# Kernel tuning notes

Hardware: AMD Instinct MI355X
Metric: run time of the kernel (lower is better)

Reference implementation:

```python
import jax, jax.numpy as jnp
import numpy as np

NUM_HEADS = 16
FUTURE_FRAMES = 2
DIM = 1024


def setup_inputs() -> dict:
    key = jax.random.key(0)
    kx, kqkv, kp, kb = jax.random.split(key, 4)
    B, T = 2, 2048
    x = jax.random.normal(kx, (B, T, DIM), dtype=jnp.float32)
    # torch Linear weights stored transposed for direct x @ W use
    w_qkv = jax.random.normal(kqkv, (DIM, 3 * DIM), dtype=jnp.float32) * (DIM ** -0.5)
    w_proj = jax.random.normal(kp, (DIM, DIM), dtype=jnp.float32) * (DIM ** -0.5)
    b_proj = jax.random.normal(kb, (DIM,), dtype=jnp.float32) * 0.01
    return {"x": x, "w_qkv": w_qkv, "w_proj": w_proj, "b_proj": b_proj}


def reference(x, w_qkv, w_proj, b_proj):
    B, T, dim = x.shape
    H = NUM_HEADS
    hd = dim // H
    qkv = x @ w_qkv                                    # (B, T, 3*dim)
    q, k, v = jnp.split(qkv, 3, axis=-1)
    # (B, H, T, hd)
    q = q.reshape(B, T, H, hd).transpose(0, 2, 1, 3)
    k = k.reshape(B, T, H, hd).transpose(0, 2, 1, 3)
    v = v.reshape(B, T, H, hd).transpose(0, 2, 1, 3)
    scale = hd ** -0.5
    scores = jnp.einsum('bhqd,bhkd->bhqk', q, k) * scale
    # banded mask: query i may attend keys j with i <= j <= i + future_frames
    i = jnp.arange(T)[:, None]
    j = jnp.arange(T)[None, :]
    allowed = (j >= i) & (j <= i + FUTURE_FRAMES)       # (T, T)
    scores = jnp.where(allowed[None, None], scores, -jnp.inf)
    attn = jax.nn.softmax(scores, axis=-1)
    out = jnp.einsum('bhqk,bhkd->bhqd', attn, v)        # (B, H, T, hd)
    out = out.transpose(0, 2, 1, 3).reshape(B, T, dim)
    return out @ w_proj + b_proj
```

## Files before the change

kernel.cpp:

```cpp
#include <hip/hip_runtime.h>
#include <hip/hip_bf16.h>
#include <cstdint>
#include <cstddef>

#define T_SEQ 2048
#define NBATCH 2
#define DIMSZ 1024
#define NHEAD 16
#define HDIM 64

typedef float f32x4 __attribute__((ext_vector_type(4)));
typedef short bf16x8 __attribute__((ext_vector_type(8)));

__device__ __forceinline__ void gld_lds16(const __hip_bfloat16* g, __hip_bfloat16* l) {
    __builtin_amdgcn_global_load_lds(
        (const __attribute__((address_space(1))) unsigned int*)g,
        (__attribute__((address_space(3))) unsigned int*)l,
        16, 0, 0);
}

__device__ __forceinline__ float bf2f(unsigned short u) {
    union { unsigned int i; float f; } c; c.i = (unsigned int)u << 16; return c.f;
}

__global__ __launch_bounds__(256) void prep(
    const float* __restrict__ x,      __hip_bfloat16* __restrict__ xb,
    const float* __restrict__ wqkv,   __hip_bfloat16* __restrict__ wqkvT,
    const float* __restrict__ wproj,  __hip_bfloat16* __restrict__ wprojT)
{
    __shared__ float tile[32][33];
    const int b = blockIdx.x;
    if (b < 4096) {
        int i = (b * 256 + threadIdx.x) * 4;
        float4 v = *(const float4*)(x + i);
        union { __hip_bfloat16 h[4]; ushort4 u; } pk;
        pk.h[0] = __hip_bfloat16(v.x); pk.h[1] = __hip_bfloat16(v.y);
        pk.h[2] = __hip_bfloat16(v.z); pk.h[3] = __hip_bfloat16(v.w);
        *(ushort4*)(xb + i) = pk.u;
        return;
    }
    const float* in; __hip_bfloat16* out; int R, C, c0, r0;
    if (b < 7168) {
        int bb = b - 4096; in = wqkv; out = wqkvT; R = 1024; C = 3072;
        c0 = (bb % 96) * 32; r0 = (bb / 96) * 32;
    } else {
        int bb = b - 7168; in = wproj; out = wprojT; R = 1024; C = 1024;
        c0 = (bb & 31) * 32; r0 = (bb >> 5) * 32;
    }
    const int tx = threadIdx.x & 31, ty = threadIdx.x >> 5;
#pragma unroll
    for (int p = 0; p < 32; p += 8)
        tile[ty + p][tx] = in[(size_t)(r0 + ty + p) * C + c0 + tx];
    __syncthreads();
#pragma unroll
    for (int p = 0; p < 32; p += 8)
        out[(size_t)(c0 + ty + p) * R + r0 + tx] = __hip_bfloat16(tile[tx][ty + p]);
}

__global__ __launch_bounds__(256) void gemm_bt_128(
    const __hip_bfloat16* __restrict__ A,
    const __hip_bfloat16* __restrict__ Bt,
    __hip_bfloat16* __restrict__ C,
    int M, int N, int K)
{
    __shared__ __align__(16) __hip_bfloat16 As[2 * 128 * 32];
    __shared__ __align__(16) __hip_bfloat16 Bs[2 * 128 * 32];

    const int tid  = threadIdx.x;
    const int wv   = tid >> 6;
    const int lane = tid & 63;
    const int bn   = blockIdx.x, bm = blockIdx.y;
    const int wm   = wv >> 1, wn = wv & 1;

    f32x4 acc[4][4] = {};

    const int srow = lane >> 2;
    const int scol = (lane & 3) * 8;

    const __hip_bfloat16* Ag = A  + (size_t)(bm * 128) * K;
    const __hip_bfloat16* Bg = Bt + (size_t)(bn * 128) * K;

    const int fm = lane & 15;
    const int fq = (lane >> 4) * 8;

    for (int kk = 0; kk < K; kk += 64) {
#pragma unroll
        for (int kh = 0; kh < 2; ++kh)
#pragma unroll
            for (int it = 0; it < 2; ++it) {
                int row = (it * 4 + wv) * 16 + srow;
                gld_lds16(Ag + (size_t)row * K + kk + kh * 32 + scol,
                          As + kh * 4096 + row * 32 + scol);
                gld_lds16(Bg + (size_t)row * K + kk + kh * 32 + scol,
                          Bs + kh * 4096 + row * 32 + scol);
            }
        __syncthreads();

#pragma unroll
        for (int kh = 0; kh < 2; ++kh) {
            bf16x8 af[4], bfr[4];
#pragma unroll
            for (int i = 0; i < 4; ++i)
                af[i] = *(const bf16x8*)(As + kh * 4096 + (wm * 64 + i * 16 + fm) * 32 + fq);
#pragma unroll
            for (int j = 0; j < 4; ++j)
                bfr[j] = *(const bf16x8*)(Bs + kh * 4096 + (wn * 64 + j * 16 + fm) * 32 + fq);
#pragma unroll
            for (int i = 0; i < 4; ++i)
#pragma unroll
                for (int j = 0; j < 4; ++j)
                    acc[i][j] = __builtin_amdgcn_mfma_f32_16x16x32_bf16(af[i], bfr[j], acc[i][j], 0, 0, 0);
        }
        __syncthreads();
    }

    const int fcol  = lane & 15;
    const int frow4 = (lane >> 4) * 4;
    const int cm0 = bm * 128 + wm * 64;
    const int cn0 = bn * 128 + wn * 64;
#pragma unroll
    for (int j = 0; j < 4; ++j) {
        int col = cn0 + j * 16 + fcol;
#pragma unroll
        for (int i = 0; i < 4; ++i)
#pragma unroll
            for (int r = 0; r < 4; ++r) {
                int row = cm0 + i * 16 + frow4 + r;
                C[(size_t)row * N + col] = __hip_bfloat16(acc[i][j][r]);
            }
    }
}

__global__ __launch_bounds__(256) void gemm_bt_64(
    const __hip_bfloat16* __restrict__ A,
    const __hip_bfloat16* __restrict__ Bt,
    const float* __restrict__ bias,
    float* __restrict__ C,
    int M, int N, int K)
{
    __shared__ __align__(16) __hip_bfloat16 As[2 * 64 * 32];
    __shared__ __align__(16) __hip_bfloat16 Bs[2 * 128 * 32];

    const int tid  = threadIdx.x;
    const int wv   = tid >> 6;
    const int lane = tid & 63;
    const int bn   = blockIdx.x, bm = blockIdx.y;
    const int wm   = wv >> 1, wn = wv & 1;

    f32x4 acc[2][4] = {};

    const int srow = lane >> 2;
    const int scol = (lane & 3) * 8;

    const __hip_bfloat16* Ag = A  + (size_t)(bm * 64) * K;
    const __hip_bfloat16* Bg = Bt + (size_t)(bn * 128) * K;

    const int fm = lane & 15;
    const int fq = (lane >> 4) * 8;

    for (int kk = 0; kk < K; kk += 64) {
#pragma unroll
        for (int kh = 0; kh < 2; ++kh) {
            {
                int row = wv * 16 + srow;
                gld_lds16(Ag + (size_t)row * K + kk + kh * 32 + scol,
                          As + kh * 2048 + row * 32 + scol);
            }
#pragma unroll
            for (int it = 0; it < 2; ++it) {
                int row = (it * 4 + wv) * 16 + srow;
                gld_lds16(Bg + (size_t)row * K + kk + kh * 32 + scol,
                          Bs + kh * 4096 + row * 32 + scol);
            }
        }
        __syncthreads();

#pragma unroll
        for (int kh = 0; kh < 2; ++kh) {
            bf16x8 af[2], bfr[4];
#pragma unroll
            for (int i = 0; i < 2; ++i)
                af[i] = *(const bf16x8*)(As + kh * 2048 + (wm * 32 + i * 16 + fm) * 32 + fq);
#pragma unroll
            for (int j = 0; j < 4; ++j)
                bfr[j] = *(const bf16x8*)(Bs + kh * 4096 + (wn * 64 + j * 16 + fm) * 32 + fq);
#pragma unroll
            for (int i = 0; i < 2; ++i)
#pragma unroll
                for (int j = 0; j < 4; ++j)
                    acc[i][j] = __builtin_amdgcn_mfma_f32_16x16x32_bf16(af[i], bfr[j], acc[i][j], 0, 0, 0);
        }
        __syncthreads();
    }

    const int fcol  = lane & 15;
    const int frow4 = (lane >> 4) * 4;
    const int cm0 = bm * 64 + wm * 32;
    const int cn0 = bn * 128 + wn * 64;
#pragma unroll
    for (int j = 0; j < 4; ++j) {
        int col = cn0 + j * 16 + fcol;
        float bv = bias[col];
#pragma unroll
        for (int i = 0; i < 2; ++i)
#pragma unroll
            for (int r = 0; r < 4; ++r) {
                int row = cm0 + i * 16 + frow4 + r;
                C[(size_t)row * N + col] = acc[i][j][r] + bv;
            }
    }
}

__global__ __launch_bounds__(256) void attn_banded(
    const __hip_bfloat16* __restrict__ qkv,
    __hip_bfloat16* __restrict__ o)
{
    const int t4 = threadIdx.x;
    const int r  = blockIdx.x;
    const int t  = r & (T_SEQ - 1);
    const size_t rb = (size_t)r * (3 * DIMSZ);
    const int d0 = t4 * 4;

    ushort4 qu = *(const ushort4*)(qkv + rb + d0);
    float q0 = bf2f(qu.x), q1 = bf2f(qu.y), q2 = bf2f(qu.z), q3 = bf2f(qu.w);

    float s[3];
    float vvx[3], vvy[3], vvz[3], vvw[3];
#pragma unroll
    for (int j = 0; j < 3; ++j) {
        bool ok = (t + j) < T_SEQ;
        size_t rbj = ok ? rb + (size_t)j * (3 * DIMSZ) : rb;
        ushort4 ku = *(const ushort4*)(qkv + rbj + DIMSZ + d0);
        ushort4 vu = *(const ushort4*)(qkv + rbj + 2 * DIMSZ + d0);
        vvx[j] = bf2f(vu.x); vvy[j] = bf2f(vu.y); vvz[j] = bf2f(vu.z); vvw[j] = bf2f(vu.w);
        float d = q0 * bf2f(ku.x) + q1 * bf2f(ku.y) + q2 * bf2f(ku.z) + q3 * bf2f(ku.w);
#pragma unroll
        for (int off = 8; off > 0; off >>= 1)
            d += __shfl_xor(d, off, 64);
        s[j] = ok ? d * 0.125f : -1e30f;
    }
    float m  = fmaxf(s[0], fmaxf(s[1], s[2]));
    float p0 = __expf(s[0] - m), p1 = __expf(s[1] - m), p2 = __expf(s[2] - m);
    float inv = 1.0f / (p0 + p1 + p2);
    union { __hip_bfloat16 h[4]; ushort4 u; } pk;
    pk.h[0] = __hip_bfloat16((p0 * vvx[0] + p1 * vvx[1] + p2 * vvx[2]) * inv);
    pk.h[1] = __hip_bfloat16((p0 * vvy[0] + p1 * vvy[1] + p2 * vvy[2]) * inv);
    pk.h[2] = __hip_bfloat16((p0 * vvz[0] + p1 * vvz[1] + p2 * vvz[2]) * inv);
    pk.h[3] = __hip_bfloat16((p0 * vvw[0] + p1 * vvw[1] + p2 * vvw[2]) * inv);
    *(ushort4*)(o + (size_t)r * DIMSZ + d0) = pk.u;
}

extern "C" void kernel_launch(void* const* d_in, const int* in_sizes, int n_in,
                              void* d_out, int out_size, void* d_ws, size_t ws_size,
                              hipStream_t stream) {
    const float* x      = (const float*)d_in[0];
    const float* w_qkv  = (const float*)d_in[1];
    const float* w_proj = (const float*)d_in[2];
    const float* b_proj = (const float*)d_in[3];
    float* out = (float*)d_out;

    const int M = NBATCH * T_SEQ;

    char* ws = (char*)d_ws;
    __hip_bfloat16* xb     = (__hip_bfloat16*)(ws);
    __hip_bfloat16* attn   = (__hip_bfloat16*)(ws);
    __hip_bfloat16* wqkvT  = (__hip_bfloat16*)(ws + (8u  << 20));
    __hip_bfloat16* wprojT = (__hip_bfloat16*)(ws + (14u << 20));
    __hip_bfloat16* qkv    = (__hip_bfloat16*)(ws + (16u << 20));

    prep<<<8192, 256, 0, stream>>>(x, xb, w_qkv, wqkvT, w_proj, wprojT);

    gemm_bt_128<<<dim3(3 * DIMSZ / 128, M / 128), 256, 0, stream>>>(
        xb, wqkvT, qkv, M, 3 * DIMSZ, DIMSZ);

    attn_banded<<<M, 256, 0, stream>>>(qkv, attn);

    gemm_bt_64<<<dim3(DIMSZ / 128, M / 64), 256, 0, stream>>>(
        attn, wprojT, b_proj, out, M, DIMSZ, DIMSZ);
}
```

Before: 145.2 us.

## Fuse all four stages into one persistent kernel with grid barriers

Replaces the four separate launches (prep, QKV GEMM, banded attention, projection GEMM) with one persistent kernel of 512 blocks that steps through the stages, separated by atomic-counter grid barriers. The QKV GEMM tile changes to 128x192 so exactly 512 tiles map onto the grid. The aim is to remove launch gaps and tail effects between kernels. The cost is spin-wait barriers that deadlock unless all 512 blocks are resident at once, reduced occupancy under the launch bound, and an extra memset launch to reset the barrier counters.

```diff
diff --git a/kernel.cpp b/kernel.cpp
--- a/kernel.cpp
+++ b/kernel.cpp
@@ -4,10 +4,8 @@
 #include <cstddef>
 
 #define T_SEQ 2048
-#define NBATCH 2
 #define DIMSZ 1024
-#define NHEAD 16
-#define HDIM 64
+#define NBLK 512
 
 typedef float f32x4 __attribute__((ext_vector_type(4)));
 typedef short bf16x8 __attribute__((ext_vector_type(8)));
@@ -23,231 +21,239 @@
     union { unsigned int i; float f; } c; c.i = (unsigned int)u << 16; return c.f;
 }
 
-__global__ __launch_bounds__(256) void prep(
+__device__ __forceinline__ void grid_barrier(int* cnt, int* gen, int target) {
+    __syncthreads();
+    if (threadIdx.x == 0) {
+        __threadfence();
+        if (atomicAdd(cnt, 1) == NBLK - 1) {
+            atomicExch(cnt, 0);
+            __threadfence();
+            atomicExch(gen, target);
+        } else {
+            while (atomicAdd(gen, 0) < target) { }
+        }
+        __threadfence();
+    }
+    __syncthreads();
+}
+
+__global__ __launch_bounds__(256, 2) void mega(
     const float* __restrict__ x,      __hip_bfloat16* __restrict__ xb,
     const float* __restrict__ wqkv,   __hip_bfloat16* __restrict__ wqkvT,
-    const float* __restrict__ wproj,  __hip_bfloat16* __restrict__ wprojT)
+    const float* __restrict__ wproj,  __hip_bfloat16* __restrict__ wprojT,
+    __hip_bfloat16* __restrict__ qkv, __hip_bfloat16* __restrict__ attn,
+    const float* __restrict__ bias,   float* __restrict__ out,
+    int* __restrict__ bar)
 {
-    __shared__ float tile[32][33];
-    const int b = blockIdx.x;
-    if (b < 4096) {
-        int i = (b * 256 + threadIdx.x) * 4;
-        float4 v = *(const float4*)(x + i);
-        union { __hip_bfloat16 h[4]; ushort4 u; } pk;
-        pk.h[0] = __hip_bfloat16(v.x); pk.h[1] = __hip_bfloat16(v.y);
-        pk.h[2] = __hip_bfloat16(v.z); pk.h[3] = __hip_bfloat16(v.w);
-        *(ushort4*)(xb + i) = pk.u;
-        return;
-    }
-    const float* in; __hip_bfloat16* out; int R, C, c0, r0;
-    if (b < 7168) {
-        int bb = b - 4096; in = wqkv; out = wqkvT; R = 1024; C = 3072;
-        c0 = (bb % 96) * 32; r0 = (bb / 96) * 32;
-    } else {
-        int bb = b - 7168; in = wproj; out = wprojT; R = 1024; C = 1024;
-        c0 = (bb & 31) * 32; r0 = (bb >> 5) * 32;
-    }
-    const int tx = threadIdx.x & 31, ty = threadIdx.x >> 5;
-#pragma unroll
-    for (int p = 0; p < 32; p += 8)
-        tile[ty + p][tx] = in[(size_t)(r0 + ty + p) * C + c0 + tx];
-    __syncthreads();
-#pragma unroll
-    for (int p = 0; p < 32; p += 8)
-        out[(size_t)(c0 + ty + p) * R + r0 + tx] = __hip_bfloat16(tile[tx][ty + p]);
-}
-
-__global__ __launch_bounds__(256) void gemm_bt_128(
-    const __hip_bfloat16* __restrict__ A,
-    const __hip_bfloat16* __restrict__ Bt,
-    __hip_bfloat16* __restrict__ C,
-    int M, int N, int K)
-{
-    __shared__ __align__(16) __hip_bfloat16 As[2 * 128 * 32];
-    __shared__ __align__(16) __hip_bfloat16 Bs[2 * 128 * 32];
-
+    __shared__ __align__(16) char smem[40960];
+    const int bid  = blockIdx.x;
     const int tid  = threadIdx.x;
     const int wv   = tid >> 6;
     const int lane = tid & 63;
-    const int bn   = blockIdx.x, bm = blockIdx.y;
-    const int wm   = wv >> 1, wn = wv & 1;
-
-    f32x4 acc[4][4] = {};
-
-    const int srow = lane >> 2;
-    const int scol = (lane & 3) * 8;
-
-    const __hip_bfloat16* Ag = A  + (size_t)(bm * 128) * K;
-    const __hip_bfloat16* Bg = Bt + (size_t)(bn * 128) * K;
-
-    const int fm = lane & 15;
-    const int fq = (lane >> 4) * 8;
-
-    for (int kk = 0; kk < K; kk += 64) {
-#pragma unroll
-        for (int kh = 0; kh < 2; ++kh)
-#pragma unroll
-            for (int it = 0; it < 2; ++it) {
-                int row = (it * 4 + wv) * 16 + srow;
-                gld_lds16(Ag + (size_t)row * K + kk + kh * 32 + scol,
-                          As + kh * 4096 + row * 32 + scol);
-                gld_lds16(Bg + (size_t)row * K + kk + kh * 32 + scol,
-                          Bs + kh * 4096 + row * 32 + scol);
-            }
-        __syncthreads();
-
-#pragma unroll
-        for (int kh = 0; kh < 2; ++kh) {
-            bf16x8 af[4], bfr[4];
+    int* cnt = bar;
+    int* gen = bar + 16;
+
+    {
+        float (*tile)[33] = (float(*)[33])smem;
+        for (int u = bid; u < 8192; u += NBLK) {
+            if (u < 4096) {
+                int i = (u * 256 + tid) * 4;
+                float4 v = *(const float4*)(x + i);
+                union { __hip_bfloat16 h[4]; ushort4 uu; } pk;
+                pk.h[0] = __hip_bfloat16(v.x); pk.h[1] = __hip_bfloat16(v.y);
+                pk.h[2] = __hip_bfloat16(v.z); pk.h[3] = __hip_bfloat16(v.w);
+                *(ushort4*)(xb + i) = pk.uu;
+            } else {
+                const float* in; __hip_bfloat16* o; int C, c0, r0;
+                if (u < 7168) {
+                    int bb = u - 4096; in = wqkv; o = wqkvT; C = 3072;
+                    c0 = (bb % 96) * 32; r0 = (bb / 96) * 32;
+                } else {
+                    int bb = u - 7168; in = wproj; o = wprojT; C = 1024;
+                    c0 = (bb & 31) * 32; r0 = (bb >> 5) * 32;
+                }
+                const int tx = tid & 31, ty = tid >> 5;
+                __syncthreads();
+#pragma unroll
+                for (int p = 0; p < 32; p += 8)
+                    tile[ty + p][tx] = in[(size_t)(r0 + ty + p) * C + c0 + tx];
+                __syncthreads();
+#pragma unroll
+                for (int p = 0; p < 32; p += 8)
+                    o[(size_t)(c0 + ty + p) * 1024 + r0 + tx] = __hip_bfloat16(tile[tx][ty + p]);
+            }
+        }
+    }
+    grid_barrier(cnt, gen, 1);
+
+    {
+        __hip_bfloat16* As = (__hip_bfloat16*)smem;
+        __hip_bfloat16* Bs = (__hip_bfloat16*)(smem + 16384);
+        const int bn = bid & 15, bm = bid >> 4;
+        const int wm = wv >> 1, wn = wv & 1;
+
+        f32x4 acc[4][6] = {};
+        const int srow = lane >> 2;
+        const int scol = (lane & 3) * 8;
+        const __hip_bfloat16* Ag = xb    + (size_t)(bm * 128) * 1024;
+        const __hip_bfloat16* Bg = wqkvT + (size_t)(bn * 192) * 1024;
+        const int fm = lane & 15;
+        const int fq = (lane >> 4) * 8;
+
+        for (int kk = 0; kk < 1024; kk += 64) {
+#pragma unroll
+            for (int kh = 0; kh < 2; ++kh) {
+#pragma unroll
+                for (int it = 0; it < 2; ++it) {
+                    int row = (it * 4 + wv) * 16 + srow;
+                    gld_lds16(Ag + (size_t)row * 1024 + kk + kh * 32 + scol,
+                              As + kh * 4096 + row * 32 + scol);
+                }
+#pragma unroll
+                for (int it = 0; it < 3; ++it) {
+                    int row = (it * 4 + wv) * 16 + srow;
+                    gld_lds16(Bg + (size_t)row * 1024 + kk + kh * 32 + scol,
+                              Bs + kh * 6144 + row * 32 + scol);
+                }
+            }
+            __syncthreads();
+
+#pragma unroll
+            for (int kh = 0; kh < 2; ++kh) {
+                bf16x8 af[4], bfr[6];
+#pragma unroll
+                for (int i = 0; i < 4; ++i)
+                    af[i] = *(const bf16x8*)(As + kh * 4096 + (wm * 64 + i * 16 + fm) * 32 + fq);
+#pragma unroll
+                for (int j = 0; j < 6; ++j)
+                    bfr[j] = *(const bf16x8*)(Bs + kh * 6144 + (wn * 96 + j * 16 + fm) * 32 + fq);
+#pragma unroll
+                for (int i = 0; i < 4; ++i)
+#pragma unroll
+                    for (int j = 0; j < 6; ++j)
+                        acc[i][j] = __builtin_amdgcn_mfma_f32_16x16x32_bf16(af[i], bfr[j], acc[i][j], 0, 0, 0);
+            }
+            __syncthreads();
+        }
+
+        const int fcol  = lane & 15;
+        const int frow4 = (lane >> 4) * 4;
+        const int cm0 = bm * 128 + wm * 64;
+        const int cn0 = bn * 192 + wn * 96;
+#pragma unroll
+        for (int j = 0; j < 6; ++j) {
+            int col = cn0 + j * 16 + fcol;
 #pragma unroll
             for (int i = 0; i < 4; ++i)
-                af[i] = *(const bf16x8*)(As + kh * 4096 + (wm * 64 + i * 16 + fm) * 32 + fq);
-#pragma unroll
-            for (int j = 0; j < 4; ++j)
-                bfr[j] = *(const bf16x8*)(Bs + kh * 4096 + (wn * 64 + j * 16 + fm) * 32 + fq);
-#pragma unroll
-            for (int i = 0; i < 4; ++i)
+#pragma unroll
+                for (int r = 0; r < 4; ++r) {
+                    int row = cm0 + i * 16 + frow4 + r;
+                    qkv[(size_t)row * 3072 + col] = __hip_bfloat16(acc[i][j][r]);
+                }
+        }
+    }
+    grid_barrier(cnt, gen, 2);
+
+    for (int r = bid; r < 4096; r += NBLK) {
+        const int t  = r & (T_SEQ - 1);
+        const size_t rb = (size_t)r * (3 * DIMSZ);
+        const int d0 = tid * 4;
+
+        ushort4 qu = *(const ushort4*)(qkv + rb + d0);
+        float q0 = bf2f(qu.x), q1 = bf2f(qu.y), q2 = bf2f(qu.z), q3 = bf2f(qu.w);
+
+        float s[3], vvx[3], vvy[3], vvz[3], vvw[3];
+#pragma unroll
+        for (int j = 0; j < 3; ++j) {
+            bool ok = (t + j) < T_SEQ;
+            size_t rbj = ok ? rb + (size_t)j * (3 * DIMSZ) : rb;
+            ushort4 ku = *(const ushort4*)(qkv + rbj + DIMSZ + d0);
+            ushort4 vu = *(const ushort4*)(qkv + rbj + 2 * DIMSZ + d0);
+            vvx[j] = bf2f(vu.x); vvy[j] = bf2f(vu.y); vvz[j] = bf2f(vu.z); vvw[j] = bf2f(vu.w);
+            float d = q0 * bf2f(ku.x) + q1 * bf2f(ku.y) + q2 * bf2f(ku.z) + q3 * bf2f(ku.w);
+#pragma unroll
+            for (int off = 8; off > 0; off >>= 1)
+                d += __shfl_xor(d, off, 64);
+            s[j] = ok ? d * 0.125f : -1e30f;
+        }
+        float m  = fmaxf(s[0], fmaxf(s[1], s[2]));
+        float p0 = __expf(s[0] - m), p1 = __expf(s[1] - m), p2 = __expf(s[2] - m);
+        float inv = 1.0f / (p0 + p1 + p2);
+        union { __hip_bfloat16 h[4]; ushort4 uu; } pk;
+        pk.h[0] = __hip_bfloat16((p0 * vvx[0] + p1 * vvx[1] + p2 * vvx[2]) * inv);
+        pk.h[1] = __hip_bfloat16((p0 * vvy[0] + p1 * vvy[1] + p2 * vvy[2]) * inv);
+        pk.h[2] = __hip_bfloat16((p0 * vvz[0] + p1 * vvz[1] + p2 * vvz[2]) * inv);
+        pk.h[3] = __hip_bfloat16((p0 * vvw[0] + p1 * vvw[1] + p2 * vvw[2]) * inv);
+        *(ushort4*)(attn + (size_t)r * DIMSZ + d0) = pk.uu;
+    }
+    grid_barrier(cnt, gen, 3);
+
+    {
+        __hip_bfloat16* As = (__hip_bfloat16*)smem;
+        __hip_bfloat16* Bs = (__hip_bfloat16*)(smem + 8192);
+        const int bn = bid & 7, bm = bid >> 3;
+        const int wm = wv >> 1, wn = wv & 1;
+
+        f32x4 acc[2][4] = {};
+        const int srow = lane >> 2;
+        const int scol = (lane & 3) * 8;
+        const __hip_bfloat16* Ag = attn   + (size_t)(bm * 64) * 1024;
+        const __hip_bfloat16* Bg = wprojT + (size_t)(bn * 128) * 1024;
+        const int fm = lane & 15;
+        const int fq = (lane >> 4) * 8;
+
+        for (int kk = 0; kk < 1024; kk += 64) {
+#pragma unroll
+            for (int kh = 0; kh < 2; ++kh) {
+                {
+                    int row = wv * 16 + srow;
+                    gld_lds16(Ag + (size_t)row * 1024 + kk + kh * 32 + scol,
+                              As + kh * 2048 + row * 32 + scol);
+                }
+#pragma unroll
+                for (int it = 0; it < 2; ++it) {
+                    int row = (it * 4 + wv) * 16 + srow;
+                    gld_lds16(Bg + (size_t)row * 1024 + kk + kh * 32 + scol,
+                              Bs + kh * 4096 + row * 32 + scol);
+                }
+            }
+            __syncthreads();
+
+#pragma unroll
+            for (int kh = 0; kh < 2; ++kh) {
+                bf16x8 af[2], bfr[4];
+#pragma unroll
+                for (int i = 0; i < 2; ++i)
+                    af[i] = *(const bf16x8*)(As + kh * 2048 + (wm * 32 + i * 16 + fm) * 32 + fq);
 #pragma unroll
                 for (int j = 0; j < 4; ++j)
-                    acc[i][j] = __builtin_amdgcn_mfma_f32_16x16x32_bf16(af[i], bfr[j], acc[i][j], 0, 0, 0);
-        }
-        __syncthreads();
-    }
-
-    const int fcol  = lane & 15;
-    const int frow4 = (lane >> 4) * 4;
-    const int cm0 = bm * 128 + wm * 64;
-    const int cn0 = bn * 128 + wn * 64;
-#pragma unroll
-    for (int j = 0; j < 4; ++j) {
-        int col = cn0 + j * 16 + fcol;
-#pragma unroll
-        for (int i = 0; i < 4; ++i)
-#pragma unroll
-            for (int r = 0; r < 4; ++r) {
-                int row = cm0 + i * 16 + frow4 + r;
-                C[(size_t)row * N + col] = __hip_bfloat16(acc[i][j][r]);
-            }
-    }
-}
-
-__global__ __launch_bounds__(256) void gemm_bt_64(
-    const __hip_bfloat16* __restrict__ A,
-    const __hip_bfloat16* __restrict__ Bt,
-    const float* __restrict__ bias,
-    float* __restrict__ C,
-    int M, int N, int K)
-{
-    __shared__ __align__(16) __hip_bfloat16 As[2 * 64 * 32];
-    __shared__ __align__(16) __hip_bfloat16 Bs[2 * 128 * 32];
-
-    const int tid  = threadIdx.x;
-    const int wv   = tid >> 6;
-    const int lane = tid & 63;
-    const int bn   = blockIdx.x, bm = blockIdx.y;
-    const int wm   = wv >> 1, wn = wv & 1;
-
-    f32x4 acc[2][4] = {};
-
-    const int srow = lane >> 2;
-    const int scol = (lane & 3) * 8;
-
-    const __hip_bfloat16* Ag = A  + (size_t)(bm * 64) * K;
-    const __hip_bfloat16* Bg = Bt + (size_t)(bn * 128) * K;
-
-    const int fm = lane & 15;
-    const int fq = (lane >> 4) * 8;
-
-    for (int kk = 0; kk < K; kk += 64) {
-#pragma unroll
-        for (int kh = 0; kh < 2; ++kh) {
-            {
-                int row = wv * 16 + srow;
-                gld_lds16(Ag + (size_t)row * K + kk + kh * 32 + scol,
-                          As + kh * 2048 + row * 32 + scol);
-            }
-#pragma unroll
-            for (int it = 0; it < 2; ++it) {
-                int row = (it * 4 + wv) * 16 + srow;
-                gld_lds16(Bg + (size_t)row * K + kk + kh * 32 + scol,
-                          Bs + kh * 4096 + row * 32 + scol);
-            }
-        }
-        __syncthreads();
-
-#pragma unroll
-        for (int kh = 0; kh < 2; ++kh) {
-            bf16x8 af[2], bfr[4];
+                    bfr[j] = *(const bf16x8*)(Bs + kh * 4096 + (wn * 64 + j * 16 + fm) * 32 + fq);
+#pragma unroll
+                for (int i = 0; i < 2; ++i)
+#pragma unroll
+                    for (int j = 0; j < 4; ++j)
+                        acc[i][j] = __builtin_amdgcn_mfma_f32_16x16x32_bf16(af[i], bfr[j], acc[i][j], 0, 0, 0);
+            }
+            __syncthreads();
+        }
+
+        const int fcol  = lane & 15;
+        const int frow4 = (lane >> 4) * 4;
+        const int cm0 = bm * 64 + wm * 32;
+        const int cn0 = bn * 128 + wn * 64;
+#pragma unroll
+        for (int j = 0; j < 4; ++j) {
+            int col = cn0 + j * 16 + fcol;
+            float bv = bias[col];
 #pragma unroll
             for (int i = 0; i < 2; ++i)
-                af[i] = *(const bf16x8*)(As + kh * 2048 + (wm * 32 + i * 16 + fm) * 32 + fq);
-#pragma unroll
-            for (int j = 0; j < 4; ++j)
-                bfr[j] = *(const bf16x8*)(Bs + kh * 4096 + (wn * 64 + j * 16 + fm) * 32 + fq);
-#pragma unroll
-            for (int i = 0; i < 2; ++i)
-#pragma unroll
-                for (int j = 0; j < 4; ++j)
-                    acc[i][j] = __builtin_amdgcn_mfma_f32_16x16x32_bf16(af[i], bfr[j], acc[i][j], 0, 0, 0);
-        }
-        __syncthreads();
-    }
-
-    const int fcol  = lane & 15;
-    const int frow4 = (lane >> 4) * 4;
-    const int cm0 = bm * 64 + wm * 32;
-    const int cn0 = bn * 128 + wn * 64;
-#pragma unroll
-    for (int j = 0; j < 4; ++j) {
-        int col = cn0 + j * 16 + fcol;
-        float bv = bias[col];
-#pragma unroll
-        for (int i = 0; i < 2; ++i)
-#pragma unroll
-            for (int r = 0; r < 4; ++r) {
-                int row = cm0 + i * 16 + frow4 + r;
-                C[(size_t)row * N + col] = acc[i][j][r] + bv;
-            }
-    }
-}
-
-__global__ __launch_bounds__(256) void attn_banded(
-    const __hip_bfloat16* __restrict__ qkv,
-    __hip_bfloat16* __restrict__ o)
-{
-    const int t4 = threadIdx.x;
-    const int r  = blockIdx.x;
-    const int t  = r & (T_SEQ - 1);
-    const size_t rb = (size_t)r * (3 * DIMSZ);
-    const int d0 = t4 * 4;
-
-    ushort4 qu = *(const ushort4*)(qkv + rb + d0);
-    float q0 = bf2f(qu.x), q1 = bf2f(qu.y), q2 = bf2f(qu.z), q3 = bf2f(qu.w);
-
-    float s[3];
-    float vvx[3], vvy[3], vvz[3], vvw[3];
-#pragma unroll
-    for (int j = 0; j < 3; ++j) {
-        bool ok = (t + j) < T_SEQ;
-        size_t rbj = ok ? rb + (size_t)j * (3 * DIMSZ) : rb;
-        ushort4 ku = *(const ushort4*)(qkv + rbj + DIMSZ + d0);
-        ushort4 vu = *(const ushort4*)(qkv + rbj + 2 * DIMSZ + d0);
-        vvx[j] = bf2f(vu.x); vvy[j] = bf2f(vu.y); vvz[j] = bf2f(vu.z); vvw[j] = bf2f(vu.w);
-        float d = q0 * bf2f(ku.x) + q1 * bf2f(ku.y) + q2 * bf2f(ku.z) + q3 * bf2f(ku.w);
-#pragma unroll
-        for (int off = 8; off > 0; off >>= 1)
-            d += __shfl_xor(d, off, 64);
-        s[j] = ok ? d * 0.125f : -1e30f;
-    }
-    float m  = fmaxf(s[0], fmaxf(s[1], s[2]));
-    float p0 = __expf(s[0] - m), p1 = __expf(s[1] - m), p2 = __expf(s[2] - m);
-    float inv = 1.0f / (p0 + p1 + p2);
-    union { __hip_bfloat16 h[4]; ushort4 u; } pk;
-    pk.h[0] = __hip_bfloat16((p0 * vvx[0] + p1 * vvx[1] + p2 * vvx[2]) * inv);
-    pk.h[1] = __hip_bfloat16((p0 * vvy[0] + p1 * vvy[1] + p2 * vvy[2]) * inv);
-    pk.h[2] = __hip_bfloat16((p0 * vvz[0] + p1 * vvz[1] + p2 * vvz[2]) * inv);
-    pk.h[3] = __hip_bfloat16((p0 * vvw[0] + p1 * vvw[1] + p2 * vvw[2]) * inv);
-    *(ushort4*)(o + (size_t)r * DIMSZ + d0) = pk.u;
+#pragma unroll
+                for (int r = 0; r < 4; ++r) {
+                    int row = cm0 + i * 16 + frow4 + r;
+                    out[(size_t)row * 1024 + col] = acc[i][j][r] + bv;
+                }
+        }
+    }
 }
 
 extern "C" void kernel_launch(void* const* d_in, const int* in_sizes, int n_in,
@@ -259,22 +265,16 @@
     const float* b_proj = (const float*)d_in[3];
     float* out = (float*)d_out;
 
-    const int M = NBATCH * T_SEQ;
-
     char* ws = (char*)d_ws;
     __hip_bfloat16* xb     = (__hip_bfloat16*)(ws);
     __hip_bfloat16* attn   = (__hip_bfloat16*)(ws);
     __hip_bfloat16* wqkvT  = (__hip_bfloat16*)(ws + (8u  << 20));
     __hip_bfloat16* wprojT = (__hip_bfloat16*)(ws + (14u << 20));
     __hip_bfloat16* qkv    = (__hip_bfloat16*)(ws + (16u << 20));
-
-    prep<<<8192, 256, 0, stream>>>(x, xb, w_qkv, wqkvT, w_proj, wprojT);
-
-    gemm_bt_128<<<dim3(3 * DIMSZ / 128, M / 128), 256, 0, stream>>>(
-        xb, wqkvT, qkv, M, 3 * DIMSZ, DIMSZ);
-
-    attn_banded<<<M, 256, 0, stream>>>(qkv, attn);
-
-    gemm_bt_64<<<dim3(DIMSZ / 128, M / 64), 256, 0, stream>>>(
-        attn, wprojT, b_proj, out, M, DIMSZ, DIMSZ);
-}
+    int* bar               = (int*)(ws + (40u << 20));
+
+    hipMemsetAsync(bar, 0, 256, stream);
+
+    mega<<<NBLK, 256, 0, stream>>>(x, xb, w_qkv, wqkvT, w_proj, wprojT,
+                                   qkv, attn, b_proj, out, bar);
+}
```

Measured after the change: 287.3 us. 97.8% more time.
